# Kernel optimization log

Measured on AMD Instinct MI355X. Metric: run time of the kernel, lower is better.

The kernel has to match this reference:

```python
import jax, jax.numpy as jnp
import numpy as np

N, P, C, M = 64, 8732, 91, 20          # batch, n_priors (SSD300), n_classes, padded objects/image
THRESHOLD = 0.5
NEG_POS_RATIO = 3
ALPHA = 1.0


def setup_inputs() -> dict:
    key = jax.random.key(0)
    k = jax.random.split(key, 7)
    predicted_locs = jax.random.normal(k[0], (N, P, 4), jnp.float32)
    predicted_scores = jax.random.normal(k[1], (N, P, C), jnp.float32)
    # ground-truth boxes in boundary (x1,y1,x2,y2) format, valid fractional coords
    xy = jax.random.uniform(k[2], (N, M, 2), minval=0.0, maxval=0.6)
    wh = jax.random.uniform(k[3], (N, M, 2), minval=0.05, maxval=0.4)
    boxes = jnp.concatenate([xy, xy + wh], axis=-1)
    labels = jax.random.randint(k[4], (N, M), 1, C).astype(jnp.int32)  # 0 = background
    # prior boxes in center-size (cx,cy,w,h) format
    cxy = jax.random.uniform(k[5], (P, 2), minval=0.05, maxval=0.95)
    pwh = jax.random.uniform(k[6], (P, 2), minval=0.05, maxval=0.3)
    priors_cxcy = jnp.concatenate([cxy, pwh], axis=-1)
    return dict(predicted_locs=predicted_locs, predicted_scores=predicted_scores,
                boxes=boxes, labels=labels, priors_cxcy=priors_cxcy)


def _iou(a, b):
    # a: (M,4) xyxy, b: (P,4) xyxy -> (M,P)
    lo = jnp.maximum(a[:, None, :2], b[None, :, :2])
    hi = jnp.minimum(a[:, None, 2:], b[None, :, 2:])
    inter = jnp.clip(hi - lo, 0.0).prod(-1)
    area_a = (a[:, 2:] - a[:, :2]).prod(-1)
    area_b = (b[:, 2:] - b[:, :2]).prod(-1)
    return inter / (area_a[:, None] + area_b[None, :] - inter)


def _xy_to_cxcy(xy):
    return jnp.concatenate([(xy[..., :2] + xy[..., 2:]) * 0.5, xy[..., 2:] - xy[..., :2]], -1)


def _cxcy_to_gcxgcy(cxcy, priors):
    g_cxcy = (cxcy[..., :2] - priors[..., :2]) / (priors[..., 2:] / 10.0)
    g_wh = jnp.log(cxcy[..., 2:] / priors[..., 2:]) * 5.0
    return jnp.concatenate([g_cxcy, g_wh], -1)


def _match_one(boxes_i, labels_i, priors_cxcy, priors_xy):
    overlap = _iou(boxes_i, priors_xy)                    # (M, P)
    ov_per_prior = overlap.max(0)                         # (P,)
    obj_per_prior = overlap.argmax(0)                     # (P,)
    prior_per_obj = overlap.argmax(1)                     # (M,)
    # force each object onto its best prior with overlap 1
    obj_per_prior = obj_per_prior.at[prior_per_obj].set(jnp.arange(M))
    ov_per_prior = ov_per_prior.at[prior_per_obj].set(1.0)
    label_per_prior = labels_i[obj_per_prior]             # (P,)
    label_per_prior = jnp.where(ov_per_prior < THRESHOLD, 0, label_per_prior)
    true_locs = _cxcy_to_gcxgcy(_xy_to_cxcy(boxes_i[obj_per_prior]), priors_cxcy)  # (P,4)
    return label_per_prior, true_locs


def reference(predicted_locs, predicted_scores, boxes, labels, priors_cxcy):
    priors_xy = jnp.concatenate([priors_cxcy[:, :2] - priors_cxcy[:, 2:] * 0.5,
                                 priors_cxcy[:, :2] + priors_cxcy[:, 2:] * 0.5], -1)
    true_classes, true_locs = jax.vmap(_match_one, in_axes=(0, 0, None, None))(
        boxes, labels, priors_cxcy, priors_xy)            # (N,P), (N,P,4)

    pos = true_classes != 0                               # (N, P)
    n_pos = pos.sum(1)                                    # (N,)
    n_pos_total = n_pos.sum().astype(jnp.float32)

    # localization: smooth L1 (beta=1), mean over positive elements
    d = predicted_locs - true_locs
    sl1 = jnp.where(jnp.abs(d) < 1.0, 0.5 * d * d, jnp.abs(d) - 0.5)   # (N,P,4)
    loc_loss = (sl1 * pos[..., None]).sum() / (n_pos_total * 4.0)

    # confidence: per-prior cross entropy
    logp = jax.nn.log_softmax(predicted_scores, axis=-1)  # (N,P,C)
    ce = -jnp.take_along_axis(logp, true_classes[..., None], axis=-1)[..., 0]  # (N,P)

    conf_loss_pos = (ce * pos).sum()
    # hard negative mining: sort negative losses desc, take 3*n_pos per image
    ce_neg = jnp.where(pos, 0.0, ce)
    ce_neg_sorted = jnp.sort(ce_neg, axis=1)[:, ::-1]     # (N,P) descending
    hard_neg = jnp.arange(P)[None, :] < (NEG_POS_RATIO * n_pos)[:, None]
    conf_loss_hard_neg = (ce_neg_sorted * hard_neg).sum()

    conf_loss = (conf_loss_pos + conf_loss_hard_neg) / n_pos_total
    return conf_loss + ALPHA * loc_loss
```

## Files before the change

### kernel.cpp

```cpp
#include <hip/hip_runtime.h>

#define NN 64
#define PP 8732
#define CC 91
#define MM 20
#define RATIO 3
#define TILES ((NN * PP) / 64)
#define BPI 8
#define CHUNK 1092

__global__ __launch_bounds__(256) void match_a(
    const float4* __restrict__ boxes4,
    const float4* __restrict__ priors4,
    float2* __restrict__ numden,
    unsigned char* __restrict__ obj8,
    unsigned long long* __restrict__ combined_part)
{
  __shared__ float bx0[MM], by0[MM], bx1[MM], by1[MM], ba[MM];
  __shared__ unsigned long long wkey[4][MM];
  const int blk = blockIdx.x, tid = threadIdx.x;
  const int wave = tid >> 6, lane = tid & 63;
  const int n = blk >> 3, part = blk & 7;
  const int c0 = part * CHUNK;
  const int cend = (c0 + CHUNK < PP) ? c0 + CHUNK : PP;

  if (tid < MM) {
    float4 b = boxes4[n * MM + tid];
    bx0[tid] = b.x; by0[tid] = b.y; bx1[tid] = b.z; by1[tid] = b.w;
    ba[tid] = (b.z - b.x) * (b.w - b.y);
  }
  __syncthreads();

  float bi[MM], bd[MM]; int bpp[MM];
#pragma unroll
  for (int m = 0; m < MM; ++m) { bi[m] = 0.0f; bd[m] = 1.0f; bpp[m] = 0; }

#pragma unroll
  for (int i = 0; i < 5; ++i) {
    int p = c0 + tid + i * 256;
    if (p < cend) {
      float4 pr = priors4[p];
      float hw = pr.z * 0.5f, hh = pr.w * 0.5f;
      float px0 = pr.x - hw, py0 = pr.y - hh, px1 = pr.x + hw, py1 = pr.y + hh;
      float pa = (px1 - px0) * (py1 - py0);
      float pi = -1.0f, pd = 1.0f; int pm = 0;
#pragma unroll
      for (int m = 0; m < MM; ++m) {
        float iw = fminf(bx1[m], px1) - fmaxf(bx0[m], px0);
        float ih = fminf(by1[m], py1) - fmaxf(by0[m], py0);
        iw = fmaxf(iw, 0.0f); ih = fmaxf(ih, 0.0f);
        float inter = iw * ih;
        float den = (ba[m] + pa) - inter;
        bool c1 = inter * pd > pi * den;
        pi = c1 ? inter : pi; pd = c1 ? den : pd; pm = c1 ? m : pm;
        bool c2 = inter * bd[m] > bi[m] * den;
        bi[m] = c2 ? inter : bi[m]; bd[m] = c2 ? den : bd[m];
        bpp[m] = c2 ? p : bpp[m];
      }
      numden[(size_t)n * PP + p] = make_float2(pi, pd);
      obj8[(size_t)n * PP + p] = (unsigned char)pm;
    }
  }

#pragma unroll
  for (int m = 0; m < MM; ++m) {
    float r = bi[m] / bd[m];
    unsigned long long key =
        ((unsigned long long)__float_as_uint(r) << 32) |
        (unsigned)(~(unsigned)bpp[m]);
#pragma unroll
    for (int d = 1; d < 64; d <<= 1) {
      unsigned long long o = __shfl_xor(key, d);
      key = (o > key) ? o : key;
    }
    if (lane == 0) wkey[wave][m] = key;
  }
  __syncthreads();
  if (tid < MM) {
    unsigned long long best = wkey[0][tid];
    unsigned long long o1 = wkey[1][tid], o2 = wkey[2][tid], o3 = wkey[3][tid];
    best = (o1 > best) ? o1 : best;
    best = (o2 > best) ? o2 : best;
    best = (o3 > best) ? o3 : best;
    combined_part[blk * MM + tid] = best;
  }
}

__global__ __launch_bounds__(256) void ce_kernel(
    const float* __restrict__ scores,
    const float4* __restrict__ pred_locs4,
    const float4* __restrict__ priors4,
    const float4* __restrict__ boxes4,
    const int* __restrict__ labels,
    const float2* __restrict__ numden,
    const unsigned char* __restrict__ obj8,
    const unsigned long long* __restrict__ combined_part,
    float* __restrict__ ce_neg,
    float4* __restrict__ partials)
{
  __shared__ float tile[64 * CC];
  __shared__ unsigned key_lo[2][MM];
  __shared__ int lbl_s[2][MM];
  __shared__ float4 box_s[2][MM];
  __shared__ float2 wpart[4];
  __shared__ int wc0[4], wc1[4];
  const int tid = threadIdx.x;
  const int base = blockIdx.x * 64;
  const int n0 = base / PP;
  const int rem0 = base - n0 * PP;

  {
    const float4* src = (const float4*)scores + (size_t)base * CC / 4;
    float4* dst = (float4*)tile;
#pragma unroll
    for (int i = 0; i < 6; ++i) {
      int idx = tid + i * 256;
      if (idx < (64 * CC) / 4) dst[idx] = src[idx];
    }
  }
  if (tid < MM) {
    const unsigned long long* cp = combined_part + (size_t)n0 * BPI * MM;
    unsigned long long best = cp[tid];
#pragma unroll
    for (int w = 1; w < BPI; ++w) {
      unsigned long long o = cp[w * MM + tid];
      best = (o > best) ? o : best;
    }
    key_lo[0][tid] = (unsigned)best;
    lbl_s[0][tid]  = labels[n0 * MM + tid];
    box_s[0][tid]  = boxes4[n0 * MM + tid];
  } else if (tid >= 64 && tid < 64 + MM) {
    int j = tid - 64, nn = (n0 + 1 < NN) ? n0 + 1 : NN - 1;
    const unsigned long long* cp = combined_part + (size_t)nn * BPI * MM;
    unsigned long long best = cp[j];
#pragma unroll
    for (int w = 1; w < BPI; ++w) {
      unsigned long long o = cp[w * MM + j];
      best = (o > best) ? o : best;
    }
    key_lo[1][j] = (unsigned)best;
    lbl_s[1][j]  = labels[nn * MM + j];
    box_s[1][j]  = boxes4[nn * MM + j];
  }
  __syncthreads();

  const int r = tid >> 2, l = tid & 3;
  const float* rowp = &tile[r * CC];
  float s = 0.0f;
  for (int c = l; c < CC; c += 4) s += __expf(rowp[c]);
  s += __shfl_xor(s, 1);
  s += __shfl_xor(s, 2);

  float cp = 0.0f, lp = 0.0f; int pos0 = 0, pos1 = 0;
  if (l == 0) {
    const int row = base + r;
    const int bn = (rem0 + r >= PP) ? 1 : 0;
    const int p = rem0 + r - bn * PP;
    float2 nd = numden[row];
    int o = obj8[row];
    int mm = -1;
    const unsigned want = ~(unsigned)p;
#pragma unroll
    for (int j = 0; j < MM; ++j) if (key_lo[bn][j] == want) mm = j;
    bool pos; int lab, sm;
    if (mm >= 0) { pos = true; sm = mm; lab = lbl_s[bn][mm]; }
    else {
      pos = !(nd.x < 0.5f * nd.y);
      sm = o; lab = pos ? lbl_s[bn][o] : 0;
    }
    float ce = __logf(s) - rowp[lab];
    if (pos) {
      cp = ce; ce_neg[row] = 0.0f;
      if (bn) pos1 = 1; else pos0 = 1;
      float4 bx = box_s[bn][sm], pr = priors4[p], pl = pred_locs4[row];
      float cx = (bx.x + bx.z) * 0.5f, cy = (bx.y + bx.w) * 0.5f;
      float w = bx.z - bx.x, h = bx.w - bx.y;
      float gx = (cx - pr.x) / (pr.z / 10.0f);
      float gy = (cy - pr.y) / (pr.w / 10.0f);
      float gz = __logf(w / pr.z) * 5.0f;
      float gw = __logf(h / pr.w) * 5.0f;
      float d, a;
      d = pl.x - gx; a = fabsf(d); lp += (a < 1.0f) ? 0.5f * d * d : a - 0.5f;
      d = pl.y - gy; a = fabsf(d); lp += (a < 1.0f) ? 0.5f * d * d : a - 0.5f;
      d = pl.z - gz; a = fabsf(d); lp += (a < 1.0f) ? 0.5f * d * d : a - 0.5f;
      d = pl.w - gw; a = fabsf(d); lp += (a < 1.0f) ? 0.5f * d * d : a - 0.5f;
    } else {
      ce_neg[row] = fmaxf(ce, 0.0f);
    }
  }

#pragma unroll
  for (int d = 1; d < 64; d <<= 1) {
    cp += __shfl_xor(cp, d); lp += __shfl_xor(lp, d);
    pos0 += __shfl_xor(pos0, d); pos1 += __shfl_xor(pos1, d);
  }
  if ((tid & 63) == 0) {
    wpart[tid >> 6] = make_float2(cp, lp);
    wc0[tid >> 6] = pos0; wc1[tid >> 6] = pos1;
  }
  __syncthreads();
  if (tid == 0) {
    float sx = 0.f, sy = 0.f; int c0 = 0, c1 = 0;
    for (int w = 0; w < 4; ++w) {
      sx += wpart[w].x; sy += wpart[w].y; c0 += wc0[w]; c1 += wc1[w];
    }
    partials[blockIdx.x] = make_float4(sx, sy, (float)c0, (float)c1);
  }
}

__global__ __launch_bounds__(256) void hardneg_kernel(
    const float* __restrict__ ce_neg, const float4* __restrict__ partials,
    float* __restrict__ hard_sum)
{
  __shared__ int wred[2][4];
  __shared__ float wredf[4];
  __shared__ int wcnt[4];
  __shared__ float wk[4];
  const int n = blockIdx.x, tid = threadIdx.x;

  unsigned uv[35];
#pragma unroll
  for (int i = 0; i < 35; ++i) {
    int p = tid + i * 256;
    uv[i] = (p < PP) ? __float_as_uint(ce_neg[(size_t)n * PP + p]) : 0u;
  }

  {
    const int bstart = (n * PP) / 64;
    const int bend = (n * PP + PP - 1) / 64;
    float kc = 0.0f;
    for (int b = bstart + tid; b <= bend; b += 256) {
      float4 pb = partials[b];
      int nb0 = (b * 64) / PP;
      if (nb0 == n)     kc += pb.z;
      if (nb0 + 1 == n) kc += pb.w;
    }
#pragma unroll
    for (int d = 1; d < 64; d <<= 1) kc += __shfl_xor(kc, d);
    if ((tid & 63) == 0) wk[tid >> 6] = kc;
    __syncthreads();
  }
  const int k = RATIO * (int)(wk[0] + wk[1] + wk[2] + wk[3] + 0.5f);

  if (k <= 0) { if (tid == 0) hard_sum[n] = 0.0f; return; }

  if (k >= PP) {
    float s = 0.0f;
#pragma unroll
    for (int i = 0; i < 35; ++i) s += __uint_as_float(uv[i]);
#pragma unroll
    for (int d = 1; d < 64; d <<= 1) s += __shfl_xor(s, d);
    if ((tid & 63) == 0) wredf[tid >> 6] = s;
    __syncthreads();
    if (tid == 0) hard_sum[n] = wredf[0] + wredf[1] + wredf[2] + wredf[3];
    return;
  }

  unsigned lo = 0u, hi = 0x7f7fffffu;
  int it = 0;
  while (lo < hi) {
    unsigned mid = lo + ((hi - lo + 1u) >> 1);
    int c = 0;
#pragma unroll
    for (int i = 0; i < 35; ++i) c += (uv[i] >= mid);
#pragma unroll
    for (int d = 1; d < 64; d <<= 1) c += __shfl_xor(c, d);
    const int buf = it & 1;
    if ((tid & 63) == 0) wred[buf][tid >> 6] = c;
    __syncthreads();
    int total = wred[buf][0] + wred[buf][1] + wred[buf][2] + wred[buf][3];
    if (total >= k) lo = mid; else hi = mid - 1u;
    ++it;
  }
  const float x = __uint_as_float(lo);

  float s = 0.0f; int c = 0;
#pragma unroll
  for (int i = 0; i < 35; ++i) {
    unsigned b = uv[i];
    if (b > lo) { s += __uint_as_float(b); ++c; }
  }
#pragma unroll
  for (int d = 1; d < 64; d <<= 1) { s += __shfl_xor(s, d); c += __shfl_xor(c, d); }
  if ((tid & 63) == 0) { wredf[tid >> 6] = s; wcnt[tid >> 6] = c; }
  __syncthreads();
  if (tid == 0) {
    float st = wredf[0] + wredf[1] + wredf[2] + wredf[3];
    int   ct = wcnt[0] + wcnt[1] + wcnt[2] + wcnt[3];
    hard_sum[n] = st + (float)(k - ct) * x;
  }
}

__global__ __launch_bounds__(256) void final_kernel(
    const float4* __restrict__ partials, const float* __restrict__ hard_sum,
    float* __restrict__ out)
{
  __shared__ float4 w4[4];
  const int tid = threadIdx.x;
  float cp = 0.0f, lp = 0.0f, np = 0.0f;
  for (int i = tid; i < TILES; i += 256) {
    float4 v = partials[i];
    cp += v.x; lp += v.y; np += v.z + v.w;
  }
  float hs = (tid < NN) ? hard_sum[tid] : 0.0f;
#pragma unroll
  for (int d = 1; d < 64; d <<= 1) {
    cp += __shfl_xor(cp, d); lp += __shfl_xor(lp, d);
    np += __shfl_xor(np, d); hs += __shfl_xor(hs, d);
  }
  if ((tid & 63) == 0) w4[tid >> 6] = make_float4(cp, lp, np, hs);
  __syncthreads();
  if (tid == 0) {
    float cpt = w4[0].x + w4[1].x + w4[2].x + w4[3].x;
    float lpt = w4[0].y + w4[1].y + w4[2].y + w4[3].y;
    float npt = w4[0].z + w4[1].z + w4[2].z + w4[3].z;
    float hst = w4[0].w + w4[1].w + w4[2].w + w4[3].w;
    out[0] = (cpt + hst) / npt + lpt / (npt * 4.0f);
  }
}

extern "C" void kernel_launch(void* const* d_in, const int* in_sizes, int n_in,
                              void* d_out, int out_size, void* d_ws, size_t ws_size,
                              hipStream_t stream) {
  const float*  pred_locs   = (const float*)d_in[0];
  const float*  pred_scores = (const float*)d_in[1];
  const float*  boxes       = (const float*)d_in[2];
  const int*    labels      = (const int*)d_in[3];
  const float*  priors      = (const float*)d_in[4];
  float* out = (float*)d_out;

  float2* numden = (float2*)d_ws;
  float4* partials = (float4*)(numden + (size_t)NN * PP);
  float*  ce_neg = (float*)(partials + TILES);
  unsigned long long* combined_part =
      (unsigned long long*)(ce_neg + (size_t)NN * PP);
  float*  hard_sum = (float*)(combined_part + NN * BPI * MM);
  unsigned char* obj8 = (unsigned char*)(hard_sum + NN);

  match_a<<<NN * BPI, 256, 0, stream>>>((const float4*)boxes,
                                        (const float4*)priors,
                                        numden, obj8, combined_part);
  ce_kernel<<<TILES, 256, 0, stream>>>(pred_scores, (const float4*)pred_locs,
                                       (const float4*)priors,
                                       (const float4*)boxes, labels,
                                       numden, obj8, combined_part,
                                       ce_neg, partials);
  hardneg_kernel<<<NN, 256, 0, stream>>>(ce_neg, partials, hard_sum);
  final_kernel<<<1, 256, 0, stream>>>(partials, hard_sum, out);
}
```

Before: 99.17 us.

## Read scores directly from global in CE kernel with larger blocks

The CE kernel no longer stages a 64-row score tile into shared memory. Each thread now reads its strided score elements directly from global memory, with four independent accumulators. Blocks grow to 512 threads covering 128 rows, which halves the block count and the partials array. The matcher stores a single IoU float instead of a numerator/denominator pair, cutting workspace traffic. The risk is that the strided direct global loads coalesce worse than the vectorized float4 staging did, and the IoU threshold test now uses a division rather than a cross-multiplied comparison.

```diff
diff --git a/kernel.cpp b/kernel.cpp
--- a/kernel.cpp
+++ b/kernel.cpp
@@ -5,19 +5,23 @@
 #define CC 91
 #define MM 20
 #define RATIO 3
-#define TILES ((NN * PP) / 64)
 #define BPI 8
 #define CHUNK 1092
+#define ROWS 128
+#define BTHR 512
+#define TILES2 ((NN * PP) / ROWS)
+
+typedef unsigned long long u64;
 
 __global__ __launch_bounds__(256) void match_a(
     const float4* __restrict__ boxes4,
     const float4* __restrict__ priors4,
-    float2* __restrict__ numden,
+    float* __restrict__ iou_out,
     unsigned char* __restrict__ obj8,
-    unsigned long long* __restrict__ combined_part)
+    u64* __restrict__ combined_part)
 {
   __shared__ float bx0[MM], by0[MM], bx1[MM], by1[MM], ba[MM];
-  __shared__ unsigned long long wkey[4][MM];
+  __shared__ u64 wkey[4][MM];
   const int blk = blockIdx.x, tid = threadIdx.x;
   const int wave = tid >> 6, lane = tid & 63;
   const int n = blk >> 3, part = blk & 7;
@@ -57,7 +61,7 @@
         bi[m] = c2 ? inter : bi[m]; bd[m] = c2 ? den : bd[m];
         bpp[m] = c2 ? p : bpp[m];
       }
-      numden[(size_t)n * PP + p] = make_float2(pi, pd);
+      iou_out[(size_t)n * PP + p] = pi / pd;
       obj8[(size_t)n * PP + p] = (unsigned char)pm;
     }
   }
@@ -65,20 +69,18 @@
 #pragma unroll
   for (int m = 0; m < MM; ++m) {
     float r = bi[m] / bd[m];
-    unsigned long long key =
-        ((unsigned long long)__float_as_uint(r) << 32) |
-        (unsigned)(~(unsigned)bpp[m]);
+    u64 key = ((u64)__float_as_uint(r) << 32) | (unsigned)(~(unsigned)bpp[m]);
 #pragma unroll
     for (int d = 1; d < 64; d <<= 1) {
-      unsigned long long o = __shfl_xor(key, d);
+      u64 o = __shfl_xor(key, d);
       key = (o > key) ? o : key;
     }
     if (lane == 0) wkey[wave][m] = key;
   }
   __syncthreads();
   if (tid < MM) {
-    unsigned long long best = wkey[0][tid];
-    unsigned long long o1 = wkey[1][tid], o2 = wkey[2][tid], o3 = wkey[3][tid];
+    u64 best = wkey[0][tid];
+    u64 o1 = wkey[1][tid], o2 = wkey[2][tid], o3 = wkey[3][tid];
     best = (o1 > best) ? o1 : best;
     best = (o2 > best) ? o2 : best;
     best = (o3 > best) ? o3 : best;
@@ -86,44 +88,38 @@
   }
 }
 
-__global__ __launch_bounds__(256) void ce_kernel(
+__global__ __launch_bounds__(BTHR) void ce_kernel(
     const float* __restrict__ scores,
     const float4* __restrict__ pred_locs4,
     const float4* __restrict__ priors4,
     const float4* __restrict__ boxes4,
     const int* __restrict__ labels,
-    const float2* __restrict__ numden,
+    const float* __restrict__ iou,
     const unsigned char* __restrict__ obj8,
-    const unsigned long long* __restrict__ combined_part,
+    const u64* __restrict__ combined_part,
     float* __restrict__ ce_neg,
     float4* __restrict__ partials)
 {
-  __shared__ float tile[64 * CC];
   __shared__ unsigned key_lo[2][MM];
   __shared__ int lbl_s[2][MM];
   __shared__ float4 box_s[2][MM];
-  __shared__ float2 wpart[4];
-  __shared__ int wc0[4], wc1[4];
+  __shared__ float4 w8[8];
   const int tid = threadIdx.x;
-  const int base = blockIdx.x * 64;
-  const int n0 = base / PP;
-  const int rem0 = base - n0 * PP;
-
-  {
-    const float4* src = (const float4*)scores + (size_t)base * CC / 4;
-    float4* dst = (float4*)tile;
-#pragma unroll
-    for (int i = 0; i < 6; ++i) {
-      int idx = tid + i * 256;
-      if (idx < (64 * CC) / 4) dst[idx] = src[idx];
-    }
-  }
+  const long base = (long)blockIdx.x * ROWS;
+  const int n0 = (int)(base / PP);
+  const int rem0 = (int)(base - (long)n0 * PP);
+  const int r = tid >> 2, l = tid & 3;
+  const long row = base + r;
+
+  const float riou = iou[row];
+  const int robj = obj8[row];
+
   if (tid < MM) {
-    const unsigned long long* cp = combined_part + (size_t)n0 * BPI * MM;
-    unsigned long long best = cp[tid];
+    const u64* cp = combined_part + (size_t)n0 * BPI * MM;
+    u64 best = cp[tid];
 #pragma unroll
     for (int w = 1; w < BPI; ++w) {
-      unsigned long long o = cp[w * MM + tid];
+      u64 o = cp[w * MM + tid];
       best = (o > best) ? o : best;
     }
     key_lo[0][tid] = (unsigned)best;
@@ -131,46 +127,54 @@
     box_s[0][tid]  = boxes4[n0 * MM + tid];
   } else if (tid >= 64 && tid < 64 + MM) {
     int j = tid - 64, nn = (n0 + 1 < NN) ? n0 + 1 : NN - 1;
-    const unsigned long long* cp = combined_part + (size_t)nn * BPI * MM;
-    unsigned long long best = cp[j];
+    const u64* cp = combined_part + (size_t)nn * BPI * MM;
+    u64 best = cp[j];
 #pragma unroll
     for (int w = 1; w < BPI; ++w) {
-      unsigned long long o = cp[w * MM + j];
+      u64 o = cp[w * MM + j];
       best = (o > best) ? o : best;
     }
     key_lo[1][j] = (unsigned)best;
     lbl_s[1][j]  = labels[nn * MM + j];
     box_s[1][j]  = boxes4[nn * MM + j];
   }
-  __syncthreads();
-
-  const int r = tid >> 2, l = tid & 3;
-  const float* rowp = &tile[r * CC];
-  float s = 0.0f;
-  for (int c = l; c < CC; c += 4) s += __expf(rowp[c]);
+
+  const float* rp = scores + (size_t)row * CC;
+  float ss0 = 0.f, ss1 = 0.f, ss2 = 0.f, ss3 = 0.f;
+#pragma unroll
+  for (int j = 0; j < 23; ++j) {
+    int c = l + 4 * j;
+    if (c < CC) {
+      float e = __expf(rp[c]);
+      if ((j & 3) == 0) ss0 += e;
+      else if ((j & 3) == 1) ss1 += e;
+      else if ((j & 3) == 2) ss2 += e;
+      else ss3 += e;
+    }
+  }
+  float s = (ss0 + ss1) + (ss2 + ss3);
   s += __shfl_xor(s, 1);
   s += __shfl_xor(s, 2);
 
-  float cp = 0.0f, lp = 0.0f; int pos0 = 0, pos1 = 0;
+  __syncthreads();
+
+  float cp_ = 0.0f, lp_ = 0.0f; int pos0 = 0, pos1 = 0;
   if (l == 0) {
-    const int row = base + r;
     const int bn = (rem0 + r >= PP) ? 1 : 0;
     const int p = rem0 + r - bn * PP;
-    float2 nd = numden[row];
-    int o = obj8[row];
-    int mm = -1;
+    int mm_ = -1;
     const unsigned want = ~(unsigned)p;
 #pragma unroll
-    for (int j = 0; j < MM; ++j) if (key_lo[bn][j] == want) mm = j;
+    for (int j = 0; j < MM; ++j) if (key_lo[bn][j] == want) mm_ = j;
     bool pos; int lab, sm;
-    if (mm >= 0) { pos = true; sm = mm; lab = lbl_s[bn][mm]; }
+    if (mm_ >= 0) { pos = true; sm = mm_; lab = lbl_s[bn][mm_]; }
     else {
-      pos = !(nd.x < 0.5f * nd.y);
-      sm = o; lab = pos ? lbl_s[bn][o] : 0;
-    }
-    float ce = __logf(s) - rowp[lab];
+      pos = !(riou < 0.5f);
+      sm = robj; lab = pos ? lbl_s[bn][robj] : 0;
+    }
+    float ce = __logf(s) - rp[lab];
     if (pos) {
-      cp = ce; ce_neg[row] = 0.0f;
+      cp_ = ce; ce_neg[row] = 0.0f;
       if (bn) pos1 = 1; else pos0 = 1;
       float4 bx = box_s[bn][sm], pr = priors4[p], pl = pred_locs4[row];
       float cx = (bx.x + bx.z) * 0.5f, cy = (bx.y + bx.w) * 0.5f;
@@ -180,10 +184,10 @@
       float gz = __logf(w / pr.z) * 5.0f;
       float gw = __logf(h / pr.w) * 5.0f;
       float d, a;
-      d = pl.x - gx; a = fabsf(d); lp += (a < 1.0f) ? 0.5f * d * d : a - 0.5f;
-      d = pl.y - gy; a = fabsf(d); lp += (a < 1.0f) ? 0.5f * d * d : a - 0.5f;
-      d = pl.z - gz; a = fabsf(d); lp += (a < 1.0f) ? 0.5f * d * d : a - 0.5f;
-      d = pl.w - gw; a = fabsf(d); lp += (a < 1.0f) ? 0.5f * d * d : a - 0.5f;
+      d = pl.x - gx; a = fabsf(d); lp_ += (a < 1.0f) ? 0.5f * d * d : a - 0.5f;
+      d = pl.y - gy; a = fabsf(d); lp_ += (a < 1.0f) ? 0.5f * d * d : a - 0.5f;
+      d = pl.z - gz; a = fabsf(d); lp_ += (a < 1.0f) ? 0.5f * d * d : a - 0.5f;
+      d = pl.w - gw; a = fabsf(d); lp_ += (a < 1.0f) ? 0.5f * d * d : a - 0.5f;
     } else {
       ce_neg[row] = fmaxf(ce, 0.0f);
     }
@@ -191,20 +195,19 @@
 
 #pragma unroll
   for (int d = 1; d < 64; d <<= 1) {
-    cp += __shfl_xor(cp, d); lp += __shfl_xor(lp, d);
+    cp_ += __shfl_xor(cp_, d); lp_ += __shfl_xor(lp_, d);
     pos0 += __shfl_xor(pos0, d); pos1 += __shfl_xor(pos1, d);
   }
-  if ((tid & 63) == 0) {
-    wpart[tid >> 6] = make_float2(cp, lp);
-    wc0[tid >> 6] = pos0; wc1[tid >> 6] = pos1;
-  }
+  if ((tid & 63) == 0)
+    w8[tid >> 6] = make_float4(cp_, lp_, (float)pos0, (float)pos1);
   __syncthreads();
   if (tid == 0) {
-    float sx = 0.f, sy = 0.f; int c0 = 0, c1 = 0;
-    for (int w = 0; w < 4; ++w) {
-      sx += wpart[w].x; sy += wpart[w].y; c0 += wc0[w]; c1 += wc1[w];
-    }
-    partials[blockIdx.x] = make_float4(sx, sy, (float)c0, (float)c1);
+    float sx = 0.f, sy = 0.f, sz = 0.f, sw = 0.f;
+#pragma unroll
+    for (int w = 0; w < 8; ++w) {
+      sx += w8[w].x; sy += w8[w].y; sz += w8[w].z; sw += w8[w].w;
+    }
+    partials[blockIdx.x] = make_float4(sx, sy, sz, sw);
   }
 }
 
@@ -226,12 +229,12 @@
   }
 
   {
-    const int bstart = (n * PP) / 64;
-    const int bend = (n * PP + PP - 1) / 64;
+    const int bstart = (n * PP) / ROWS;
+    const int bend = (n * PP + PP - 1) / ROWS;
     float kc = 0.0f;
     for (int b = bstart + tid; b <= bend; b += 256) {
       float4 pb = partials[b];
-      int nb0 = (b * 64) / PP;
+      int nb0 = (b * ROWS) / PP;
       if (nb0 == n)     kc += pb.z;
       if (nb0 + 1 == n) kc += pb.w;
     }
@@ -298,7 +301,7 @@
   __shared__ float4 w4[4];
   const int tid = threadIdx.x;
   float cp = 0.0f, lp = 0.0f, np = 0.0f;
-  for (int i = tid; i < TILES; i += 256) {
+  for (int i = tid; i < TILES2; i += 256) {
     float4 v = partials[i];
     cp += v.x; lp += v.y; np += v.z + v.w;
   }
@@ -329,22 +332,21 @@
   const float*  priors      = (const float*)d_in[4];
   float* out = (float*)d_out;
 
-  float2* numden = (float2*)d_ws;
-  float4* partials = (float4*)(numden + (size_t)NN * PP);
-  float*  ce_neg = (float*)(partials + TILES);
-  unsigned long long* combined_part =
-      (unsigned long long*)(ce_neg + (size_t)NN * PP);
+  float* iou_ws = (float*)d_ws;
+  float4* partials = (float4*)(iou_ws + (size_t)NN * PP);
+  float*  ce_neg = (float*)(partials + TILES2);
+  u64* combined_part = (u64*)(ce_neg + (size_t)NN * PP);
   float*  hard_sum = (float*)(combined_part + NN * BPI * MM);
   unsigned char* obj8 = (unsigned char*)(hard_sum + NN);
 
   match_a<<<NN * BPI, 256, 0, stream>>>((const float4*)boxes,
                                         (const float4*)priors,
-                                        numden, obj8, combined_part);
-  ce_kernel<<<TILES, 256, 0, stream>>>(pred_scores, (const float4*)pred_locs,
-                                       (const float4*)priors,
-                                       (const float4*)boxes, labels,
-                                       numden, obj8, combined_part,
-                                       ce_neg, partials);
+                                        iou_ws, obj8, combined_part);
+  ce_kernel<<<TILES2, BTHR, 0, stream>>>(pred_scores, (const float4*)pred_locs,
+                                         (const float4*)priors,
+                                         (const float4*)boxes, labels,
+                                         iou_ws, obj8, combined_part,
+                                         ce_neg, partials);
   hardneg_kernel<<<NN, 256, 0, stream>>>(ce_neg, partials, hard_sum);
   final_kernel<<<1, 256, 0, stream>>>(partials, hard_sum, out);
 }
```

Result: faster. 84.86 us (-14.4%).
